# Kernel optimization log

Hardware: AMD Instinct MI355X
Metric: run time of the kernel (lower is better)

The kernel has to match this reference:

```python
import jax, jax.numpy as jnp
import numpy as np

DIM = 256
FOCAL_LEVEL = 3
FOCAL_WINDOW = 3
FOCAL_FACTOR = 2


def _dwconv(x, k):
    # depthwise conv, SAME padding via explicit k//2 (matches ZeroPadding2D + VALID Conv2D)
    p = k.shape[0] // 2
    return jax.lax.conv_general_dilated(
        x, k, window_strides=(1, 1), padding=[(p, p), (p, p)],
        dimension_numbers=("NHWC", "HWIO", "NHWC"), feature_group_count=DIM)


def setup_inputs() -> dict:
    key = jax.random.key(0)
    ks = jax.random.split(key, 8)
    B, H, W = 32, 64, 64
    C_out = 2 * DIM + (FOCAL_LEVEL + 1)  # 516
    x = jax.random.normal(ks[0], (B, H, W, DIM), jnp.float32)
    w_init = jax.random.normal(ks[1], (DIM, C_out), jnp.float32) * 0.02
    b_init = jnp.zeros((C_out,), jnp.float32)
    kernels = []
    for i in range(FOCAL_LEVEL):
        s = FOCAL_FACTOR * i + FOCAL_WINDOW  # 3, 5, 7
        kernels.append(jax.random.normal(ks[2 + i], (s, s, 1, DIM), jnp.float32) * 0.02)
    w_mod = jax.random.normal(ks[5], (DIM, DIM), jnp.float32) * 0.02
    b_mod = jnp.zeros((DIM,), jnp.float32)
    w_proj = jax.random.normal(ks[6], (DIM, DIM), jnp.float32) * 0.02
    b_proj = jnp.zeros((DIM,), jnp.float32)
    return {"x": x, "w_init": w_init, "b_init": b_init,
            "k0": kernels[0], "k1": kernels[1], "k2": kernels[2],
            "w_mod": w_mod, "b_mod": b_mod, "w_proj": w_proj, "b_proj": b_proj}


def reference(x, w_init, b_init, k0, k1, k2, w_mod, b_mod, w_proj, b_proj):
    gelu = lambda t: jax.nn.gelu(t, approximate=False)
    x_proj = x @ w_init + b_init                       # [B,H,W,2*DIM+L+1]
    query = x_proj[..., :DIM]
    context = x_proj[..., DIM:2 * DIM]
    gates = jnp.clip(x_proj[..., 2 * DIM:], -1.0, 1.0)  # [B,H,W,L+1]

    ctx = gelu(_dwconv(context, k0))
    context_all = ctx * gates[..., 0:1]
    for idx, k in enumerate((k1, k2), start=1):
        ctx = gelu(_dwconv(ctx, k))
        context_all = context_all + ctx * gates[..., idx:idx + 1]

    context_global = jnp.tanh(jnp.mean(ctx, axis=(1, 2), keepdims=True))  # GAP+tanh
    context_all = context_all + context_global * gates[..., FOCAL_LEVEL:]

    modulator = context_all @ w_mod + b_mod            # 1x1 conv == per-pixel dense
    query = jnp.clip(query, -100.0, 100.0)
    modulator = jnp.clip(modulator, -100.0, 100.0)
    out = (query * modulator) @ w_proj + b_proj        # dropout identity (eval)
    return out
```

## Files before the change

### kernel.cpp

```cpp
#include <hip/hip_runtime.h>
#include <math.h>

#define DIMC 256
#define CO   516
#define NB   32
#define NH   64
#define NW   64
#define NPIX (NB*NH*NW)
#define PITCH 264
#define CP    76
#define CROWS 72

typedef short short8 __attribute__((ext_vector_type(8)));
typedef float floatx4 __attribute__((ext_vector_type(4)));
typedef unsigned short us4 __attribute__((ext_vector_type(4)));

__device__ __forceinline__ float gelu_f(float x) {
    return 0.5f * x * (1.0f + erff(x * 0.7071067811865476f));
}
__device__ __forceinline__ float clip100(float v) {
    return fminf(100.f, fmaxf(-100.f, v));
}
__device__ __forceinline__ void split2(float x, unsigned short& h, unsigned short& l) {
    unsigned int xb = __float_as_uint(x);
    unsigned int hb = (xb + 0x7fffu + ((xb >> 16) & 1u)) & 0xffff0000u;
    h = (unsigned short)(hb >> 16);
    float r = x - __uint_as_float(hb);
    unsigned int rb = __float_as_uint(r);
    l = (unsigned short)((rb + 0x7fffu + ((rb >> 16) & 1u)) >> 16);
}

__global__ __launch_bounds__(256) void k_prep(const float* __restrict__ w_init,
                                              const float* __restrict__ w_mod,
                                              const float* __restrict__ w_proj,
                                              unsigned short* wiF_h, unsigned short* wiF_l,
                                              unsigned short* wmF_h, unsigned short* wmF_l,
                                              unsigned short* wpF_h, unsigned short* wpF_l,
                                              unsigned short* wgF_h, unsigned short* wgF_l) {
    const int n = blockIdx.x;
    const int k = threadIdx.x;
    const int kki = k >> 5, quad = (k >> 3) & 3, j = k & 7;
    unsigned short h, l;
    if (n < 1024) {
        const int nn = (n < 512) ? n : (n < 768 ? n - 512 : n - 768);
        const int g = nn >> 6, in_ = (nn >> 4) & 3, l15 = nn & 15;
        const size_t idx = ((size_t)((g * 8 + kki) * 4 + in_) * 64 + quad * 16 + l15) * 8 + j;
        if (n < 512) {
            split2(w_init[k * CO + n], h, l);
            wiF_h[idx] = h; wiF_l[idx] = l;
        } else if (n < 768) {
            split2(w_mod[k * 256 + nn], h, l);
            wmF_h[idx] = h; wmF_l[idx] = l;
        } else {
            split2(w_proj[k * 256 + nn], h, l);
            wpF_h[idx] = h; wpF_l[idx] = l;
        }
    } else {
        const int nn = n - 1024;
        const float v = (nn < 4) ? w_init[k * CO + 512 + nn] : 0.f;
        split2(v, h, l);
        const size_t idx = ((size_t)kki * 64 + quad * 16 + nn) * 8 + j;
        wgF_h[idx] = h; wgF_l[idx] = l;
    }
}

__global__ __launch_bounds__(256) void k_init_mfma(const float* __restrict__ x,
                                                   const unsigned short* __restrict__ wiF_h,
                                                   const unsigned short* __restrict__ wiF_l,
                                                   const unsigned short* __restrict__ wgF_h,
                                                   const unsigned short* __restrict__ wgF_l,
                                                   const float* __restrict__ b_init,
                                                   float* __restrict__ qout,
                                                   float* __restrict__ ctxp,
                                                   float* __restrict__ gates) {
    __shared__ unsigned short Ah[16384];
    __shared__ unsigned short Al[16384];
    const int t = threadIdx.x;
    const int wv = t >> 6, lane = t & 63;
    const int l15 = lane & 15, quad = lane >> 4;
    const long tile = blockIdx.x;
    const long p0 = tile * 64;
    const int bb = (int)(p0 >> 12);
    const int pl = (int)(p0 & 4095);

    {
        const float* xr = x + (size_t)(p0 + wv * 16 + l15) * 256 + quad * 8;
        #pragma unroll
        for (int kki = 0; kki < 8; ++kki) {
            const float4 v0 = *(const float4*)&xr[kki * 32];
            const float4 v1 = *(const float4*)&xr[kki * 32 + 4];
            short8 hh, ll;
            unsigned short h, l;
            split2(v0.x, h, l); hh[0] = (short)h; ll[0] = (short)l;
            split2(v0.y, h, l); hh[1] = (short)h; ll[1] = (short)l;
            split2(v0.z, h, l); hh[2] = (short)h; ll[2] = (short)l;
            split2(v0.w, h, l); hh[3] = (short)h; ll[3] = (short)l;
            split2(v1.x, h, l); hh[4] = (short)h; ll[4] = (short)l;
            split2(v1.y, h, l); hh[5] = (short)h; ll[5] = (short)l;
            split2(v1.z, h, l); hh[6] = (short)h; ll[6] = (short)l;
            split2(v1.w, h, l); hh[7] = (short)h; ll[7] = (short)l;
            const int o = ((wv * 8 + kki) * 64 + lane) * 8;
            *(short8*)&Ah[o] = hh;
            *(short8*)&Al[o] = ll;
        }
    }
    __syncthreads();

    for (int half = 0; half < 2; ++half) {
        const int g = half * 4 + wv;
        const unsigned short* Bh = wiF_h + (size_t)g * 16384;
        const unsigned short* Bl = wiF_l + (size_t)g * 16384;
        floatx4 acc[4][4];
        #pragma unroll
        for (int im = 0; im < 4; ++im)
            #pragma unroll
            for (int in_ = 0; in_ < 4; ++in_)
                acc[im][in_] = (floatx4){0.f, 0.f, 0.f, 0.f};

        #pragma unroll
        for (int kki = 0; kki < 8; ++kki) {
            short8 ah[4], al[4], bh[4], bl[4];
            #pragma unroll
            for (int in_ = 0; in_ < 4; ++in_) {
                const int o = ((kki * 4 + in_) * 64 + lane) * 8;
                bh[in_] = *(const short8*)&Bh[o];
                bl[in_] = *(const short8*)&Bl[o];
            }
            #pragma unroll
            for (int im = 0; im < 4; ++im) {
                const int o = ((im * 8 + kki) * 64 + lane) * 8;
                ah[im] = *(const short8*)&Ah[o];
                al[im] = *(const short8*)&Al[o];
            }
            #pragma unroll
            for (int im = 0; im < 4; ++im)
                #pragma unroll
                for (int in_ = 0; in_ < 4; ++in_) {
                    acc[im][in_] = __builtin_amdgcn_mfma_f32_16x16x32_bf16(ah[im], bh[in_], acc[im][in_], 0, 0, 0);
                    acc[im][in_] = __builtin_amdgcn_mfma_f32_16x16x32_bf16(ah[im], bl[in_], acc[im][in_], 0, 0, 0);
                    acc[im][in_] = __builtin_amdgcn_mfma_f32_16x16x32_bf16(al[im], bh[in_], acc[im][in_], 0, 0, 0);
                }
        }

        if (half == 0) {
            #pragma unroll
            for (int in_ = 0; in_ < 4; ++in_) {
                const int col = wv * 64 + in_ * 16 + l15;
                const float bi = b_init[col];
                #pragma unroll
                for (int im = 0; im < 4; ++im)
                    #pragma unroll
                    for (int r = 0; r < 4; ++r) {
                        const int row = im * 16 + quad * 4 + r;
                        qout[(p0 + row) * 256 + col] = acc[im][in_][r] + bi;
                    }
            }
        } else {
            #pragma unroll
            for (int in_ = 0; in_ < 4; ++in_) {
                const int col = wv * 64 + in_ * 16 + l15;
                const float bi = b_init[256 + col];
                #pragma unroll
                for (int im = 0; im < 4; ++im) {
                    float4 o;
                    o.x = acc[im][in_][0] + bi;
                    o.y = acc[im][in_][1] + bi;
                    o.z = acc[im][in_][2] + bi;
                    o.w = acc[im][in_][3] + bi;
                    *(float4*)&ctxp[((size_t)bb * 256 + col) * 4096 + pl + im * 16 + quad * 4] = o;
                }
            }
        }
    }

    {
        floatx4 gacc = (floatx4){0.f, 0.f, 0.f, 0.f};
        #pragma unroll
        for (int kki = 0; kki < 8; ++kki) {
            const int oa = ((wv * 8 + kki) * 64 + lane) * 8;
            const short8 a_h = *(const short8*)&Ah[oa];
            const short8 a_l = *(const short8*)&Al[oa];
            const int ob = (kki * 64 + lane) * 8;
            const short8 b_h = *(const short8*)&wgF_h[ob];
            const short8 b_l = *(const short8*)&wgF_l[ob];
            gacc = __builtin_amdgcn_mfma_f32_16x16x32_bf16(a_h, b_h, gacc, 0, 0, 0);
            gacc = __builtin_amdgcn_mfma_f32_16x16x32_bf16(a_h, b_l, gacc, 0, 0, 0);
            gacc = __builtin_amdgcn_mfma_f32_16x16x32_bf16(a_l, b_h, gacc, 0, 0, 0);
        }
        if (l15 < 4) {
            const float bi = b_init[512 + l15];
            #pragma unroll
            for (int r = 0; r < 4; ++r) {
                const int row = wv * 16 + quad * 4 + r;
                gates[(p0 + row) * 4 + l15] = fminf(1.f, fmaxf(-1.f, gacc[r] + bi));
            }
        }
    }
}

template<int KS>
__device__ __forceinline__ void conv_level(const float* __restrict__ kwp,
                                           const float* __restrict__ I,
                                           int ry0, int cx0, float v[16]) {
    constexpr int P = KS / 2;
    constexpr int RWIN = 4 + 2 * P;
    float wk[KS * KS];
    #pragma unroll
    for (int i = 0; i < KS * KS; ++i) wk[i] = kwp[i * 256];

    float4 rb[RWIN][3];
    #pragma unroll
    for (int r = 0; r < 2 * P; ++r) {
        const int base = (ry0 + r - P + 4) * CP + cx0;
        rb[r][0] = *(const float4*)&I[base];
        rb[r][1] = *(const float4*)&I[base + 4];
        rb[r][2] = *(const float4*)&I[base + 8];
    }
    #pragma unroll
    for (int j = 0; j < 4; ++j) {
        {
            const int r = j + 2 * P;
            const int base = (ry0 + r - P + 4) * CP + cx0;
            rb[r][0] = *(const float4*)&I[base];
            rb[r][1] = *(const float4*)&I[base + 4];
            rb[r][2] = *(const float4*)&I[base + 8];
        }
        float s0 = 0.f, s1 = 0.f, s2 = 0.f, s3 = 0.f;
        #pragma unroll
        for (int dy = 0; dy < KS; ++dy) {
            const float* rw = (const float*)&rb[j + dy][0];
            #pragma unroll
            for (int dx = 0; dx < KS; ++dx) {
                const float wgt = wk[dy * KS + dx];
                s0 += rw[4 - P + 0 + dx] * wgt;
                s1 += rw[4 - P + 1 + dx] * wgt;
                s2 += rw[4 - P + 2 + dx] * wgt;
                s3 += rw[4 - P + 3 + dx] * wgt;
            }
        }
        v[j * 4 + 0] = gelu_f(s0);
        v[j * 4 + 1] = gelu_f(s1);
        v[j * 4 + 2] = gelu_f(s2);
        v[j * 4 + 3] = gelu_f(s3);
    }
}

__global__ __launch_bounds__(256) void k_conv_fused(const float* __restrict__ ctxp,
                                                    const float* __restrict__ k0,
                                                    const float* __restrict__ k1,
                                                    const float* __restrict__ k2,
                                                    const float* __restrict__ gates,
                                                    float* __restrict__ c_allp) {
    __shared__ float X[CROWS * CP];
    __shared__ float Y[CROWS * CP];
    const int t = threadIdx.x;
    const int bc = blockIdx.x;
    const int b = bc >> 8, c = bc & 255;
    const float* src = ctxp + (size_t)bc * 4096;

    for (int i = t; i < CROWS * CP; i += 256) { X[i] = 0.f; Y[i] = 0.f; }
    __syncthreads();
    #pragma unroll
    for (int i = 0; i < 4; ++i) {
        const int p = i * 1024 + t * 4;
        const float4 vv = *(const float4*)&src[p];
        *(float4*)&X[((p >> 6) + 4) * CP + (p & 63) + 4] = vv;
    }
    __syncthreads();

    const int px = t & 15, py = t >> 4;
    const int cx0 = px * 4, ry0 = py * 4;
    const float* gbase = gates + (size_t)b * 4096 * 4;

    float acc[16], v[16];

    conv_level<3>(k0 + c, X, ry0, cx0, v);
    #pragma unroll
    for (int j = 0; j < 4; ++j) {
        *(float4*)&Y[(ry0 + j + 4) * CP + cx0 + 4] = *(float4*)&v[j * 4];
        #pragma unroll
        for (int i2 = 0; i2 < 4; ++i2)
            acc[j * 4 + i2] = v[j * 4 + i2] * gbase[((ry0 + j) * 64 + cx0 + i2) * 4 + 0];
    }
    __syncthreads();

    conv_level<5>(k1 + c, Y, ry0, cx0, v);
    #pragma unroll
    for (int j = 0; j < 4; ++j) {
        *(float4*)&X[(ry0 + j + 4) * CP + cx0 + 4] = *(float4*)&v[j * 4];
        #pragma unroll
        for (int i2 = 0; i2 < 4; ++i2)
            acc[j * 4 + i2] += v[j * 4 + i2] * gbase[((ry0 + j) * 64 + cx0 + i2) * 4 + 1];
    }
    __syncthreads();

    conv_level<7>(k2 + c, X, ry0, cx0, v);
    float vsum = 0.f;
    #pragma unroll
    for (int j = 0; j < 4; ++j)
        #pragma unroll
        for (int i2 = 0; i2 < 4; ++i2) {
            acc[j * 4 + i2] += v[j * 4 + i2] * gbase[((ry0 + j) * 64 + cx0 + i2) * 4 + 2];
            vsum += v[j * 4 + i2];
        }

    __syncthreads();
    X[t] = vsum;
    __syncthreads();
    if (t < 64) {
        float s = X[t] + X[t + 64] + X[t + 128] + X[t + 192];
        #pragma unroll
        for (int off = 32; off >= 1; off >>= 1)
            s += __shfl_down(s, off, 64);
        if (t == 0) X[0] = tanhf(s * (1.f / 4096.f));
    }
    __syncthreads();
    const float gl = X[0];

    float* dst = c_allp + (size_t)bc * 4096;
    #pragma unroll
    for (int j = 0; j < 4; ++j) {
        float4 o;
        o.x = acc[j * 4 + 0] + gl * gbase[((ry0 + j) * 64 + cx0 + 0) * 4 + 3];
        o.y = acc[j * 4 + 1] + gl * gbase[((ry0 + j) * 64 + cx0 + 1) * 4 + 3];
        o.z = acc[j * 4 + 2] + gl * gbase[((ry0 + j) * 64 + cx0 + 2) * 4 + 3];
        o.w = acc[j * 4 + 3] + gl * gbase[((ry0 + j) * 64 + cx0 + 3) * 4 + 3];
        *(float4*)&dst[(ry0 + j) * 64 + cx0] = o;
    }
}

__global__ __launch_bounds__(256) void k_final_mfma(float* qout,
                                                    const float* __restrict__ c_allp,
                                                    const unsigned short* __restrict__ wmF_h,
                                                    const unsigned short* __restrict__ wmF_l,
                                                    const unsigned short* __restrict__ wpF_h,
                                                    const unsigned short* __restrict__ wpF_l,
                                                    const float* __restrict__ b_mod,
                                                    const float* __restrict__ b_proj) {
    __shared__ unsigned short Ah[64 * PITCH];
    __shared__ unsigned short Al[64 * PITCH];
    const int t = threadIdx.x;
    const long p0 = (long)blockIdx.x * 64;
    const int b = (int)(p0 >> 12);
    const int pl = (int)(p0 & 4095);

    {
        const float* src = c_allp + ((size_t)b * 256 + t) * 4096 + pl;
        #pragma unroll
        for (int i = 0; i < 16; ++i) {
            const float4 vv = *(const float4*)&src[i * 4];
            unsigned short h, l;
            split2(vv.x, h, l); Ah[(i*4+0)*PITCH + t] = h; Al[(i*4+0)*PITCH + t] = l;
            split2(vv.y, h, l); Ah[(i*4+1)*PITCH + t] = h; Al[(i*4+1)*PITCH + t] = l;
            split2(vv.z, h, l); Ah[(i*4+2)*PITCH + t] = h; Al[(i*4+2)*PITCH + t] = l;
            split2(vv.w, h, l); Ah[(i*4+3)*PITCH + t] = h; Al[(i*4+3)*PITCH + t] = l;
        }
    }
    __syncthreads();

    const int wv = t >> 6, lane = t & 63;
    const int l15 = lane & 15, quad = lane >> 4;
    const int ncol0 = wv * 64;
    const unsigned short* BmH = wmF_h + (size_t)wv * 16384;
    const unsigned short* BmL = wmF_l + (size_t)wv * 16384;
    const unsigned short* BpH = wpF_h + (size_t)wv * 16384;
    const unsigned short* BpL = wpF_l + (size_t)wv * 16384;

    floatx4 acc[4][4];
    #pragma unroll
    for (int im = 0; im < 4; ++im)
        #pragma unroll
        for (int in_ = 0; in_ < 4; ++in_)
            acc[im][in_] = (floatx4){0.f, 0.f, 0.f, 0.f};

    #pragma unroll
    for (int kki = 0; kki < 8; ++kki) {
        short8 ah[4], al[4], bh[4], bl[4];
        #pragma unroll
        for (int in_ = 0; in_ < 4; ++in_) {
            const int o = ((kki * 4 + in_) * 64 + lane) * 8;
            bh[in_] = *(const short8*)&BmH[o];
            bl[in_] = *(const short8*)&BmL[o];
        }
        #pragma unroll
        for (int im = 0; im < 4; ++im) {
            const int off = (im * 16 + l15) * PITCH + kki * 32 + quad * 8;
            ah[im] = *(const short8*)&Ah[off];
            al[im] = *(const short8*)&Al[off];
        }
        #pragma unroll
        for (int im = 0; im < 4; ++im)
            #pragma unroll
            for (int in_ = 0; in_ < 4; ++in_) {
                acc[im][in_] = __builtin_amdgcn_mfma_f32_16x16x32_bf16(ah[im], bh[in_], acc[im][in_], 0, 0, 0);
                acc[im][in_] = __builtin_amdgcn_mfma_f32_16x16x32_bf16(ah[im], bl[in_], acc[im][in_], 0, 0, 0);
                acc[im][in_] = __builtin_amdgcn_mfma_f32_16x16x32_bf16(al[im], bh[in_], acc[im][in_], 0, 0, 0);
            }
    }
    __syncthreads();

    #pragma unroll
    for (int in_ = 0; in_ < 4; ++in_) {
        const int col = ncol0 + in_ * 16 + l15;
        const float bm = b_mod[col];
        #pragma unroll
        for (int im = 0; im < 4; ++im)
            #pragma unroll
            for (int r = 0; r < 4; ++r) {
                const int row = im * 16 + quad * 4 + r;
                const float m = clip100(acc[im][in_][r] + bm);
                const float qv = clip100(qout[(p0 + row) * 256 + col]);
                unsigned short h, l;
                split2(qv * m, h, l);
                Ah[row * PITCH + col] = h;
                Al[row * PITCH + col] = l;
            }
    }
    __syncthreads();

    #pragma unroll
    for (int im = 0; im < 4; ++im)
        #pragma unroll
        for (int in_ = 0; in_ < 4; ++in_)
            acc[im][in_] = (floatx4){0.f, 0.f, 0.f, 0.f};

    #pragma unroll
    for (int kki = 0; kki < 8; ++kki) {
        short8 ah[4], al[4], bh[4], bl[4];
        #pragma unroll
        for (int in_ = 0; in_ < 4; ++in_) {
            const int o = ((kki * 4 + in_) * 64 + lane) * 8;
            bh[in_] = *(const short8*)&BpH[o];
            bl[in_] = *(const short8*)&BpL[o];
        }
        #pragma unroll
        for (int im = 0; im < 4; ++im) {
            const int off = (im * 16 + l15) * PITCH + kki * 32 + quad * 8;
            ah[im] = *(const short8*)&Ah[off];
            al[im] = *(const short8*)&Al[off];
        }
        #pragma unroll
        for (int im = 0; im < 4; ++im)
            #pragma unroll
            for (int in_ = 0; in_ < 4; ++in_) {
                acc[im][in_] = __builtin_amdgcn_mfma_f32_16x16x32_bf16(ah[im], bh[in_], acc[im][in_], 0, 0, 0);
                acc[im][in_] = __builtin_amdgcn_mfma_f32_16x16x32_bf16(ah[im], bl[in_], acc[im][in_], 0, 0, 0);
                acc[im][in_] = __builtin_amdgcn_mfma_f32_16x16x32_bf16(al[im], bh[in_], acc[im][in_], 0, 0, 0);
            }
    }

    #pragma unroll
    for (int in_ = 0; in_ < 4; ++in_) {
        const int col = ncol0 + in_ * 16 + l15;
        const float bp = b_proj[col];
        #pragma unroll
        for (int im = 0; im < 4; ++im)
            #pragma unroll
            for (int r = 0; r < 4; ++r) {
                const int row = im * 16 + quad * 4 + r;
                qout[(p0 + row) * 256 + col] = acc[im][in_][r] + bp;
            }
    }
}

extern "C" void kernel_launch(void* const* d_in, const int* in_sizes, int n_in,
                              void* d_out, int out_size, void* d_ws, size_t ws_size,
                              hipStream_t stream) {
    const float* x      = (const float*)d_in[0];
    const float* w_init = (const float*)d_in[1];
    const float* b_init = (const float*)d_in[2];
    const float* k0     = (const float*)d_in[3];
    const float* k1     = (const float*)d_in[4];
    const float* k2     = (const float*)d_in[5];
    const float* w_mod  = (const float*)d_in[6];
    const float* b_mod  = (const float*)d_in[7];
    const float* w_proj = (const float*)d_in[8];
    const float* b_proj = (const float*)d_in[9];
    float* qout = (float*)d_out;

    float* ws = (float*)d_ws;
    const long NP = (long)NPIX * DIMC;
    float* ctxp    = ws;
    float* c_allp  = ws + NP;
    float* gates   = ws + 2 * NP;
    unsigned short* wiF_h = (unsigned short*)(gates + (long)NPIX * 4);
    unsigned short* wiF_l = wiF_h + 512 * 256;
    unsigned short* wmF_h = wiF_l + 512 * 256;
    unsigned short* wmF_l = wmF_h + 256 * 256;
    unsigned short* wpF_h = wmF_l + 256 * 256;
    unsigned short* wpF_l = wpF_h + 256 * 256;
    unsigned short* wgF_h = wpF_l + 256 * 256;
    unsigned short* wgF_l = wgF_h + 16 * 256;

    k_prep<<<1040, 256, 0, stream>>>(w_init, w_mod, w_proj,
                                     wiF_h, wiF_l, wmF_h, wmF_l, wpF_h, wpF_l,
                                     wgF_h, wgF_l);
    k_init_mfma<<<NPIX / 64, 256, 0, stream>>>(x, wiF_h, wiF_l,
                                               wgF_h, wgF_l, b_init,
                                               qout, ctxp, gates);
    k_conv_fused<<<NB * 256, 256, 0, stream>>>(ctxp, k0, k1, k2, gates, c_allp);
    k_final_mfma<<<NPIX / 64, 256, 0, stream>>>(qout, c_allp,
                                                wmF_h, wmF_l, wpF_h, wpF_l,
                                                b_mod, b_proj);
}
```

Before: 942.3 us.

## Halve init LDS via two-stage K split; double conv block threads

The init GEMM kernel now stages x in two K halves through a half-size shared buffer. It computes the query, context and gate accumulations together in one pass instead of running separate passes over the full tile. This lowers LDS use so more blocks can be resident, at the cost of holding two accumulator sets in registers, which may raise VGPR pressure. The conv kernel switches to 512 threads with 2 rows per thread instead of 4, which halves per-thread registers and adds parallelism but increases halo reloads per output.

```diff
diff --git a/kernel.cpp b/kernel.cpp
--- a/kernel.cpp
+++ b/kernel.cpp
@@ -73,8 +73,8 @@
                                                    float* __restrict__ qout,
                                                    float* __restrict__ ctxp,
                                                    float* __restrict__ gates) {
-    __shared__ unsigned short Ah[16384];
-    __shared__ unsigned short Al[16384];
+    __shared__ unsigned short Ah[8192];
+    __shared__ unsigned short Al[8192];
     const int t = threadIdx.x;
     const int wv = t >> 6, lane = t & 63;
     const int l15 = lane & 15, quad = lane >> 4;
@@ -83,117 +83,130 @@
     const int bb = (int)(p0 >> 12);
     const int pl = (int)(p0 & 4095);
 
-    {
-        const float* xr = x + (size_t)(p0 + wv * 16 + l15) * 256 + quad * 8;
-        #pragma unroll
-        for (int kki = 0; kki < 8; ++kki) {
+    const float* xr = x + (size_t)(p0 + wv * 16 + l15) * 256 + quad * 8;
+    const unsigned short* BqH = wiF_h + (size_t)wv * 16384;
+    const unsigned short* BqL = wiF_l + (size_t)wv * 16384;
+    const unsigned short* BcH = wiF_h + (size_t)(4 + wv) * 16384;
+    const unsigned short* BcL = wiF_l + (size_t)(4 + wv) * 16384;
+
+    floatx4 accq[4][4], accc[4][4], gacc;
+    #pragma unroll
+    for (int im = 0; im < 4; ++im)
+        #pragma unroll
+        for (int in_ = 0; in_ < 4; ++in_) {
+            accq[im][in_] = (floatx4){0.f, 0.f, 0.f, 0.f};
+            accc[im][in_] = (floatx4){0.f, 0.f, 0.f, 0.f};
+        }
+    gacc = (floatx4){0.f, 0.f, 0.f, 0.f};
+
+    #pragma unroll
+    for (int h = 0; h < 2; ++h) {
+        #pragma unroll
+        for (int kk2 = 0; kk2 < 4; ++kk2) {
+            const int kki = h * 4 + kk2;
             const float4 v0 = *(const float4*)&xr[kki * 32];
             const float4 v1 = *(const float4*)&xr[kki * 32 + 4];
             short8 hh, ll;
-            unsigned short h, l;
-            split2(v0.x, h, l); hh[0] = (short)h; ll[0] = (short)l;
-            split2(v0.y, h, l); hh[1] = (short)h; ll[1] = (short)l;
-            split2(v0.z, h, l); hh[2] = (short)h; ll[2] = (short)l;
-            split2(v0.w, h, l); hh[3] = (short)h; ll[3] = (short)l;
-            split2(v1.x, h, l); hh[4] = (short)h; ll[4] = (short)l;
-            split2(v1.y, h, l); hh[5] = (short)h; ll[5] = (short)l;
-            split2(v1.z, h, l); hh[6] = (short)h; ll[6] = (short)l;
-            split2(v1.w, h, l); hh[7] = (short)h; ll[7] = (short)l;
-            const int o = ((wv * 8 + kki) * 64 + lane) * 8;
+            unsigned short hs, ls;
+            split2(v0.x, hs, ls); hh[0] = (short)hs; ll[0] = (short)ls;
+            split2(v0.y, hs, ls); hh[1] = (short)hs; ll[1] = (short)ls;
+            split2(v0.z, hs, ls); hh[2] = (short)hs; ll[2] = (short)ls;
+            split2(v0.w, hs, ls); hh[3] = (short)hs; ll[3] = (short)ls;
+            split2(v1.x, hs, ls); hh[4] = (short)hs; ll[4] = (short)ls;
+            split2(v1.y, hs, ls); hh[5] = (short)hs; ll[5] = (short)ls;
+            split2(v1.z, hs, ls); hh[6] = (short)hs; ll[6] = (short)ls;
+            split2(v1.w, hs, ls); hh[7] = (short)hs; ll[7] = (short)ls;
+            const int o = ((wv * 4 + kk2) * 64 + lane) * 8;
             *(short8*)&Ah[o] = hh;
             *(short8*)&Al[o] = ll;
         }
-    }
-    __syncthreads();
-
-    for (int half = 0; half < 2; ++half) {
-        const int g = half * 4 + wv;
-        const unsigned short* Bh = wiF_h + (size_t)g * 16384;
-        const unsigned short* Bl = wiF_l + (size_t)g * 16384;
-        floatx4 acc[4][4];
-        #pragma unroll
-        for (int im = 0; im < 4; ++im)
-            #pragma unroll
-            for (int in_ = 0; in_ < 4; ++in_)
-                acc[im][in_] = (floatx4){0.f, 0.f, 0.f, 0.f};
-
-        #pragma unroll
-        for (int kki = 0; kki < 8; ++kki) {
+        __syncthreads();
+
+        #pragma unroll
+        for (int kk2 = 0; kk2 < 4; ++kk2) {
+            const int kki = h * 4 + kk2;
             short8 ah[4], al[4], bh[4], bl[4];
+            #pragma unroll
+            for (int im = 0; im < 4; ++im) {
+                const int o = ((im * 4 + kk2) * 64 + lane) * 8;
+                ah[im] = *(const short8*)&Ah[o];
+                al[im] = *(const short8*)&Al[o];
+            }
             #pragma unroll
             for (int in_ = 0; in_ < 4; ++in_) {
                 const int o = ((kki * 4 + in_) * 64 + lane) * 8;
-                bh[in_] = *(const short8*)&Bh[o];
-                bl[in_] = *(const short8*)&Bl[o];
-            }
-            #pragma unroll
-            for (int im = 0; im < 4; ++im) {
-                const int o = ((im * 8 + kki) * 64 + lane) * 8;
-                ah[im] = *(const short8*)&Ah[o];
-                al[im] = *(const short8*)&Al[o];
+                bh[in_] = *(const short8*)&BqH[o];
+                bl[in_] = *(const short8*)&BqL[o];
             }
             #pragma unroll
             for (int im = 0; im < 4; ++im)
                 #pragma unroll
                 for (int in_ = 0; in_ < 4; ++in_) {
-                    acc[im][in_] = __builtin_amdgcn_mfma_f32_16x16x32_bf16(ah[im], bh[in_], acc[im][in_], 0, 0, 0);
-                    acc[im][in_] = __builtin_amdgcn_mfma_f32_16x16x32_bf16(ah[im], bl[in_], acc[im][in_], 0, 0, 0);
-                    acc[im][in_] = __builtin_amdgcn_mfma_f32_16x16x32_bf16(al[im], bh[in_], acc[im][in_], 0, 0, 0);
+                    accq[im][in_] = __builtin_amdgcn_mfma_f32_16x16x32_bf16(ah[im], bh[in_], accq[im][in_], 0, 0, 0);
+                    accq[im][in_] = __builtin_amdgcn_mfma_f32_16x16x32_bf16(ah[im], bl[in_], accq[im][in_], 0, 0, 0);
+                    accq[im][in_] = __builtin_amdgcn_mfma_f32_16x16x32_bf16(al[im], bh[in_], accq[im][in_], 0, 0, 0);
                 }
-        }
-
-        if (half == 0) {
             #pragma unroll
             for (int in_ = 0; in_ < 4; ++in_) {
-                const int col = wv * 64 + in_ * 16 + l15;
-                const float bi = b_init[col];
+                const int o = ((kki * 4 + in_) * 64 + lane) * 8;
+                bh[in_] = *(const short8*)&BcH[o];
+                bl[in_] = *(const short8*)&BcL[o];
+            }
+            #pragma unroll
+            for (int im = 0; im < 4; ++im)
                 #pragma unroll
-                for (int im = 0; im < 4; ++im)
-                    #pragma unroll
-                    for (int r = 0; r < 4; ++r) {
-                        const int row = im * 16 + quad * 4 + r;
-                        qout[(p0 + row) * 256 + col] = acc[im][in_][r] + bi;
-                    }
-            }
-        } else {
-            #pragma unroll
-            for (int in_ = 0; in_ < 4; ++in_) {
-                const int col = wv * 64 + in_ * 16 + l15;
-                const float bi = b_init[256 + col];
-                #pragma unroll
-                for (int im = 0; im < 4; ++im) {
-                    float4 o;
-                    o.x = acc[im][in_][0] + bi;
-                    o.y = acc[im][in_][1] + bi;
-                    o.z = acc[im][in_][2] + bi;
-                    o.w = acc[im][in_][3] + bi;
-                    *(float4*)&ctxp[((size_t)bb * 256 + col) * 4096 + pl + im * 16 + quad * 4] = o;
+                for (int in_ = 0; in_ < 4; ++in_) {
+                    accc[im][in_] = __builtin_amdgcn_mfma_f32_16x16x32_bf16(ah[im], bh[in_], accc[im][in_], 0, 0, 0);
+                    accc[im][in_] = __builtin_amdgcn_mfma_f32_16x16x32_bf16(ah[im], bl[in_], accc[im][in_], 0, 0, 0);
+                    accc[im][in_] = __builtin_amdgcn_mfma_f32_16x16x32_bf16(al[im], bh[in_], accc[im][in_], 0, 0, 0);
                 }
-            }
-        }
-    }
-
-    {
-        floatx4 gacc = (floatx4){0.f, 0.f, 0.f, 0.f};
-        #pragma unroll
-        for (int kki = 0; kki < 8; ++kki) {
-            const int oa = ((wv * 8 + kki) * 64 + lane) * 8;
-            const short8 a_h = *(const short8*)&Ah[oa];
-            const short8 a_l = *(const short8*)&Al[oa];
-            const int ob = (kki * 64 + lane) * 8;
-            const short8 b_h = *(const short8*)&wgF_h[ob];
-            const short8 b_l = *(const short8*)&wgF_l[ob];
-            gacc = __builtin_amdgcn_mfma_f32_16x16x32_bf16(a_h, b_h, gacc, 0, 0, 0);
-            gacc = __builtin_amdgcn_mfma_f32_16x16x32_bf16(a_h, b_l, gacc, 0, 0, 0);
-            gacc = __builtin_amdgcn_mfma_f32_16x16x32_bf16(a_l, b_h, gacc, 0, 0, 0);
-        }
-        if (l15 < 4) {
-            const float bi = b_init[512 + l15];
+            {
+                const int oga = ((wv * 4 + kk2) * 64 + lane) * 8;
+                const short8 gah = *(const short8*)&Ah[oga];
+                const short8 gal = *(const short8*)&Al[oga];
+                const int ob = (kki * 64 + lane) * 8;
+                const short8 gbh = *(const short8*)&wgF_h[ob];
+                const short8 gbl = *(const short8*)&wgF_l[ob];
+                gacc = __builtin_amdgcn_mfma_f32_16x16x32_bf16(gah, gbh, gacc, 0, 0, 0);
+                gacc = __builtin_amdgcn_mfma_f32_16x16x32_bf16(gah, gbl, gacc, 0, 0, 0);
+                gacc = __builtin_amdgcn_mfma_f32_16x16x32_bf16(gal, gbh, gacc, 0, 0, 0);
+            }
+        }
+        if (h == 0) __syncthreads();
+    }
+
+    #pragma unroll
+    for (int in_ = 0; in_ < 4; ++in_) {
+        const int col = wv * 64 + in_ * 16 + l15;
+        const float bi = b_init[col];
+        #pragma unroll
+        for (int im = 0; im < 4; ++im)
             #pragma unroll
             for (int r = 0; r < 4; ++r) {
-                const int row = wv * 16 + quad * 4 + r;
-                gates[(p0 + row) * 4 + l15] = fminf(1.f, fmaxf(-1.f, gacc[r] + bi));
-            }
+                const int row = im * 16 + quad * 4 + r;
+                qout[(p0 + row) * 256 + col] = accq[im][in_][r] + bi;
+            }
+    }
+    #pragma unroll
+    for (int in_ = 0; in_ < 4; ++in_) {
+        const int col = wv * 64 + in_ * 16 + l15;
+        const float bi = b_init[256 + col];
+        #pragma unroll
+        for (int im = 0; im < 4; ++im) {
+            float4 o;
+            o.x = accc[im][in_][0] + bi;
+            o.y = accc[im][in_][1] + bi;
+            o.z = accc[im][in_][2] + bi;
+            o.w = accc[im][in_][3] + bi;
+            *(float4*)&ctxp[((size_t)bb * 256 + col) * 4096 + pl + im * 16 + quad * 4] = o;
+        }
+    }
+    if (l15 < 4) {
+        const float bi = b_init[512 + l15];
+        #pragma unroll
+        for (int r = 0; r < 4; ++r) {
+            const int row = wv * 16 + quad * 4 + r;
+            gates[(p0 + row) * 4 + l15] = fminf(1.f, fmaxf(-1.f, gacc[r] + bi));
         }
     }
 }
@@ -201,9 +214,9 @@
 template<int KS>
 __device__ __forceinline__ void conv_level(const float* __restrict__ kwp,
                                            const float* __restrict__ I,
-                                           int ry0, int cx0, float v[16]) {
+                                           int ry0, int cx0, float v[8]) {
     constexpr int P = KS / 2;
-    constexpr int RWIN = 4 + 2 * P;
+    constexpr int RWIN = 2 + 2 * P;
     float wk[KS * KS];
     #pragma unroll
     for (int i = 0; i < KS * KS; ++i) wk[i] = kwp[i * 256];
@@ -217,7 +230,7 @@
         rb[r][2] = *(const float4*)&I[base + 8];
     }
     #pragma unroll
-    for (int j = 0; j < 4; ++j) {
+    for (int j = 0; j < 2; ++j) {
         {
             const int r = j + 2 * P;
             const int base = (ry0 + r - P + 4) * CP + cx0;
@@ -245,7 +258,7 @@
     }
 }
 
-__global__ __launch_bounds__(256) void k_conv_fused(const float* __restrict__ ctxp,
+__global__ __launch_bounds__(512) void k_conv_fused(const float* __restrict__ ctxp,
                                                     const float* __restrict__ k0,
                                                     const float* __restrict__ k1,
                                                     const float* __restrict__ k2,
@@ -258,25 +271,25 @@
     const int b = bc >> 8, c = bc & 255;
     const float* src = ctxp + (size_t)bc * 4096;
 
-    for (int i = t; i < CROWS * CP; i += 256) { X[i] = 0.f; Y[i] = 0.f; }
-    __syncthreads();
-    #pragma unroll
-    for (int i = 0; i < 4; ++i) {
-        const int p = i * 1024 + t * 4;
+    for (int i = t; i < CROWS * CP; i += 512) { X[i] = 0.f; Y[i] = 0.f; }
+    __syncthreads();
+    #pragma unroll
+    for (int i = 0; i < 2; ++i) {
+        const int p = i * 2048 + t * 4;
         const float4 vv = *(const float4*)&src[p];
         *(float4*)&X[((p >> 6) + 4) * CP + (p & 63) + 4] = vv;
     }
     __syncthreads();
 
     const int px = t & 15, py = t >> 4;
-    const int cx0 = px * 4, ry0 = py * 4;
+    const int cx0 = px * 4, ry0 = py * 2;
     const float* gbase = gates + (size_t)b * 4096 * 4;
 
-    float acc[16], v[16];
+    float acc[8], v[8];
 
     conv_level<3>(k0 + c, X, ry0, cx0, v);
     #pragma unroll
-    for (int j = 0; j < 4; ++j) {
+    for (int j = 0; j < 2; ++j) {
         *(float4*)&Y[(ry0 + j + 4) * CP + cx0 + 4] = *(float4*)&v[j * 4];
         #pragma unroll
         for (int i2 = 0; i2 < 4; ++i2)
@@ -286,7 +299,7 @@
 
     conv_level<5>(k1 + c, Y, ry0, cx0, v);
     #pragma unroll
-    for (int j = 0; j < 4; ++j) {
+    for (int j = 0; j < 2; ++j) {
         *(float4*)&X[(ry0 + j + 4) * CP + cx0 + 4] = *(float4*)&v[j * 4];
         #pragma unroll
         for (int i2 = 0; i2 < 4; ++i2)
@@ -297,7 +310,7 @@
     conv_level<7>(k2 + c, X, ry0, cx0, v);
     float vsum = 0.f;
     #pragma unroll
-    for (int j = 0; j < 4; ++j)
+    for (int j = 0; j < 2; ++j)
         #pragma unroll
         for (int i2 = 0; i2 < 4; ++i2) {
             acc[j * 4 + i2] += v[j * 4 + i2] * gbase[((ry0 + j) * 64 + cx0 + i2) * 4 + 2];
@@ -308,7 +321,9 @@
     X[t] = vsum;
     __syncthreads();
     if (t < 64) {
-        float s = X[t] + X[t + 64] + X[t + 128] + X[t + 192];
+        float s = 0.f;
+        #pragma unroll
+        for (int k = 0; k < 8; ++k) s += X[t + 64 * k];
         #pragma unroll
         for (int off = 32; off >= 1; off >>= 1)
             s += __shfl_down(s, off, 64);
@@ -319,7 +334,7 @@
 
     float* dst = c_allp + (size_t)bc * 4096;
     #pragma unroll
-    for (int j = 0; j < 4; ++j) {
+    for (int j = 0; j < 2; ++j) {
         float4 o;
         o.x = acc[j * 4 + 0] + gl * gbase[((ry0 + j) * 64 + cx0 + 0) * 4 + 3];
         o.y = acc[j * 4 + 1] + gl * gbase[((ry0 + j) * 64 + cx0 + 1) * 4 + 3];
@@ -498,7 +513,7 @@
     k_init_mfma<<<NPIX / 64, 256, 0, stream>>>(x, wiF_h, wiF_l,
                                                wgF_h, wgF_l, b_init,
                                                qout, ctxp, gates);
-    k_conv_fused<<<NB * 256, 256, 0, stream>>>(ctxp, k0, k1, k2, gates, c_allp);
+    k_conv_fused<<<NB * 256, 512, 0, stream>>>(ctxp, k0, k1, k2, gates, c_allp);
     k_final_mfma<<<NPIX / 64, 256, 0, stream>>>(qout, c_allp,
                                                 wmF_h, wmF_l, wpF_h, wpF_l,
                                                 b_mod, b_proj);
```

After: 866.0 us. 1.09x faster.
